# Performance work log

Hardware: AMD Instinct MI355X
Metric: run time of the kernel (lower is better)

Reference implementation:

```python
import jax, jax.numpy as jnp
import numpy as np

C = 256
C8 = C // 8
B, H, W = 4, 64, 64


def setup_inputs() -> dict:
    key = jax.random.key(0)
    ks = jax.random.split(key, 10)
    s = lambda fan_in: 1.0 / np.sqrt(fan_in)
    return {
        "x": jax.random.normal(ks[0], (B, C, H, W), dtype=jnp.float32),
        "conv_w": jax.random.normal(ks[1], (C8, C), dtype=jnp.float32) * s(C),
        "conv_b": jax.random.normal(ks[2], (C8,), dtype=jnp.float32) * 0.01,
        "q_w": jax.random.normal(ks[3], (C8, C8), dtype=jnp.float32) * s(C8),
        "q_b": jax.random.normal(ks[4], (C8,), dtype=jnp.float32) * 0.01,
        "k_w": jax.random.normal(ks[5], (C8, C8), dtype=jnp.float32) * s(C8),
        "k_b": jax.random.normal(ks[6], (C8,), dtype=jnp.float32) * 0.01,
        "v_w": jax.random.normal(ks[7], (C, C8), dtype=jnp.float32) * s(C8),
        "v_b": jax.random.normal(ks[8], (C,), dtype=jnp.float32) * 0.01,
        "gamma": jax.random.normal(ks[9], (1,), dtype=jnp.float32) * 0.1,
    }


def reference(x, conv_w, conv_b, q_w, q_b, k_w, k_b, v_w, v_b, gamma):
    b, c, h, w = x.shape
    hw = h * w
    # 1x1 convs are channel-mixing matmuls over flattened spatial dims
    xf = x.reshape(b, c, hw)                                   # [B, C, HW]
    proj = jnp.einsum('dc,bcn->bdn', conv_w, xf) + conv_b[None, :, None]   # [B, C8, HW]
    q = jnp.einsum('ed,bdn->bne', q_w, proj) + q_b[None, None, :]          # [B, HW, C8]
    k = jnp.einsum('ed,bdn->ben', k_w, proj) + k_b[None, :, None]          # [B, C8, HW]
    v = jnp.einsum('cd,bdn->bcn', v_w, proj) + v_b[None, :, None]          # [B, C, HW]
    attn = jax.nn.softmax(jnp.einsum('bne,bem->bnm', q, k), axis=-1)       # [B, HW, HW]
    out = jnp.einsum('bcm,bnm->bcn', v, attn)                              # [B, C, HW]
    out = out.reshape(b, c, h, w)
    return gamma[0] * out + x
```

## Files before the change

### kernel.cpp

```cpp
#include <hip/hip_runtime.h>
#include <hip/hip_bf16.h>
#include <stdint.h>

#define B_   4
#define C_   256
#define C8_  32
#define HW_  4096
#define ROWS_ 320
#define MS_  4
#define L2E  1.4426950408889634f

typedef __attribute__((ext_vector_type(8)))  short  short8;
typedef __attribute__((ext_vector_type(8)))  ushort us8;
typedef __attribute__((ext_vector_type(2)))  float  f32x2;
typedef __attribute__((ext_vector_type(16))) float  f32x16;

#define WT_OFF    0
#define BALL_OFF  (256*320*4)
#define Q_OFF     (BALL_OFF + 1280)
#define KT_OFF    (Q_OFF  + B_*HW_*C8_*2)
#define V_OFF     (KT_OFF + B_*HW_*C8_*2)
#define PACC_OFF  (V_OFF  + B_*C_*HW_*2)
#define LPART_OFF (PACC_OFF + (size_t)MS_*B_*C_*HW_*2)

__device__ __forceinline__ ushort f2bf(float f) {
    union { float f; uint32_t u; } v; v.f = f;
    uint32_t u = v.u;
    uint32_t r = u + 0x7fffu + ((u >> 16) & 1u);
    return (ushort)(r >> 16);
}
__device__ __forceinline__ uint32_t pktr(float lo, float hi) {
    union { float f; uint32_t u; } a, b; a.f = lo; b.f = hi;
    return __builtin_amdgcn_perm(b.u, a.u, 0x07060302u);
}
__device__ __forceinline__ uint32_t fexp2_pk(float s0, float s1, f32x2& e01) {
    f32x2 s = {s0, s1};
    f32x2 y = __builtin_elementwise_fma(s, (f32x2)(8388608.0f),
                                        (f32x2)(1064992506.0f));
    y = __builtin_elementwise_max(y, (f32x2)(0.0f));
    union { int i; float f; } c0, c1;
    c0.i = (int)y.x;  c1.i = (int)y.y;
    e01.x = c0.f;  e01.y = c1.f;
    return __builtin_amdgcn_perm((uint32_t)c1.i, (uint32_t)c0.i, 0x07060302u);
}

__global__ __launch_bounds__(256) void k_setup(
    const float* __restrict__ conv_w, const float* __restrict__ conv_b,
    const float* __restrict__ q_w, const float* __restrict__ q_b,
    const float* __restrict__ k_w, const float* __restrict__ k_b,
    const float* __restrict__ v_w, const float* __restrict__ v_b,
    ushort* __restrict__ wbf, float* __restrict__ ball)
{
    int r = blockIdx.x;
    int c = threadIdx.x;
    const float* wrow;
    float bias;
    if (r < 32)       { wrow = q_w + r*32;      bias = q_b[r];      }
    else if (r < 64)  { wrow = k_w + (r-32)*32; bias = k_b[r-32];   }
    else              { wrow = v_w + (r-64)*32; bias = v_b[r-64];   }
    float acc = 0.f;
    #pragma unroll
    for (int d = 0; d < 32; ++d) acc += wrow[d] * conv_w[d*C_ + c];
    float scale = (r < 32) ? L2E : 1.0f;
    int lanew = (r & 31) + 32*((c >> 3) & 1);
    int fidx  = (c >> 4)*10 + (r >> 5);
    wbf[fidx*512 + lanew*8 + (c & 7)] = f2bf(acc * scale);
    if (c == 0) {
        float bb = bias;
        #pragma unroll
        for (int d = 0; d < 32; ++d) bb += wrow[d] * conv_b[d];
        ball[r] = bb * scale;
    }
}

__global__ __launch_bounds__(320) void k_qkv(
    const float* __restrict__ x, const ushort* __restrict__ wbf,
    const float* __restrict__ ball,
    ushort* __restrict__ qg, ushort* __restrict__ ktg, ushort* __restrict__ vg)
{
    __shared__ float  xt[256*32];
    __shared__ ushort tr[5][32*40];

    int blk = blockIdx.x;
    int b  = blk >> 7;
    int nt = blk & 127;
    int n0 = nt * 32;
    int t = threadIdx.x;
    int w = t >> 6, lane = t & 63;
    int l31 = lane & 31, h = lane >> 5;

    const float* xsrc = x + (size_t)b*C_*HW_ + n0;
    if (w < 4) {
        #pragma unroll
        for (int i = 0; i < 8; ++i) {
            int chunk = w*8 + i;
            const float* src = xsrc + (size_t)(chunk*8 + (lane >> 3))*HW_
                               + (lane & 7)*4;
            __builtin_amdgcn_global_load_lds(
                (const __attribute__((address_space(1))) uint32_t*)src,
                (__attribute__((address_space(3))) uint32_t*)&xt[chunk*256],
                16, 0, 0);
        }
    }
    __syncthreads();

    f32x16 acc[2];
    acc[0] = (f32x16)(0.f);
    acc[1] = (f32x16)(0.f);

    #pragma unroll 4
    for (int kc = 0; kc < 16; ++kc) {
        short8 a0 = *(const short8*)(wbf + (kc*10 + w*2    )*512 + lane*8);
        short8 a1 = *(const short8*)(wbf + (kc*10 + w*2 + 1)*512 + lane*8);
        float xv[8];
        #pragma unroll
        for (int j = 0; j < 8; ++j)
            xv[j] = xt[kc*512 + (h*8 + j)*32 + l31];
        union { uint32_t d[4]; short8 s8; } bf;
        #pragma unroll
        for (int j2 = 0; j2 < 4; ++j2) bf.d[j2] = pktr(xv[2*j2], xv[2*j2+1]);
        acc[0] = __builtin_amdgcn_mfma_f32_32x32x16_bf16(a0, bf.s8, acc[0], 0, 0, 0);
        acc[1] = __builtin_amdgcn_mfma_f32_32x32x16_bf16(a1, bf.s8, acc[1], 0, 0, 0);
    }

    #pragma unroll
    for (int mi = 0; mi < 2; ++mi) {
        int rowb = w*64 + mi*32;
        bool isQK = (rowb < 64);
        #pragma unroll
        for (int r = 0; r < 16; ++r) {
            int roff = (r & 3) + 8*(r >> 2) + 4*h;
            ushort bv = f2bf(acc[mi][r] + ball[rowb + roff]);
            int ad = isQK ? (l31*40 + roff) : (roff*40 + l31);
            tr[w][ad] = bv;
        }
        __syncthreads();
        #pragma unroll
        for (int f = 0; f < 2; ++f) {
            us8 frag = *(const us8*)(&tr[w][l31*40 + f*16 + h*8]);
            if (isQK) {
                ushort* dstb = (rowb == 0) ? qg : ktg;
                size_t ad = ((size_t)((b*128 + nt)*2 + f) << 9) + lane*8;
                *(us8*)(dstb + ad) = frag;
            } else {
                int cblk = (rowb - 64) >> 5;
                int mb = nt*2 + f;
                size_t ad = ((size_t)((b*8 + cblk)*256 + mb) << 9) + lane*8;
                *(us8*)(vg + ad) = frag;
            }
        }
        __syncthreads();
    }
}

__global__ __launch_bounds__(512, 4) void k_attn(
    const ushort* __restrict__ qg, const ushort* __restrict__ ktg,
    const ushort* __restrict__ vg,
    ushort* __restrict__ pacc, float* __restrict__ lpart)
{
    __shared__ ushort v_lds[2][16*512];
    __shared__ ushort kt_lds[2][4*512];

    int blk = blockIdx.x;
    int ms = blk & 3;
    int cs = (blk >> 2) & 1;
    int qb = (blk >> 3) & 15;
    int b  = blk >> 7;
    int t = threadIdx.x;
    int w = t >> 6, lane = t & 63;
    int l31 = lane & 31, h = lane >> 5;
    int mbase = ms*1024;

    short8 qf[2];
    #pragma unroll
    for (int ks = 0; ks < 2; ++ks)
        qf[ks] = *(const short8*)(qg
            + ((size_t)((b*128 + qb*8 + w)*2 + ks) << 9) + lane*8);

    f32x16 acc[4];
    #pragma unroll
    for (int j = 0; j < 4; ++j) acc[j] = (f32x16)(0.f);
    f32x2 lacc0 = {0.f, 0.f};
    f32x2 lacc1 = {0.f, 0.f};

    #define STAGE(buf, m0)                                                          \
    {                                                                               \
        _Pragma("unroll")                                                           \
        for (int ff = 0; ff < 2; ++ff) {                                            \
            int f = w*2 + ff;                                                       \
            int cfr = f >> 2, mf = f & 3;                                           \
            const ushort* src = vg + ((size_t)((b*8 + cs*4 + cfr)*256               \
                                 + ((m0) >> 4) + mf) << 9) + lane*8;                \
            __builtin_amdgcn_global_load_lds(                                       \
                (const __attribute__((address_space(1))) uint32_t*)src,             \
                (__attribute__((address_space(3))) uint32_t*)&v_lds[buf][f*512],    \
                16, 0, 0);                                                          \
        }                                                                           \
        if (w < 4) {                                                                \
            const ushort* src = ktg + ((size_t)((b*128 + ((m0) >> 5) + (w >> 1))*2  \
                                 + (w & 1)) << 9) + lane*8;                         \
            __builtin_amdgcn_global_load_lds(                                       \
                (const __attribute__((address_space(1))) uint32_t*)src,             \
                (__attribute__((address_space(3))) uint32_t*)&kt_lds[buf][w*512],   \
                16, 0, 0);                                                          \
        }                                                                           \
    }

    #define PMERGE(uu, lo8, hi8)                                                    \
    {                                                                               \
        union { uint32_t d[4]; short8 s8; } fe_, fo_;                               \
        auto r02 = __builtin_amdgcn_permlane32_swap((int)uu[0], (int)uu[2], false, false); \
        auto r13 = __builtin_amdgcn_permlane32_swap((int)uu[1], (int)uu[3], false, false); \
        auto r46 = __builtin_amdgcn_permlane32_swap((int)uu[4], (int)uu[6], false, false); \
        auto r57 = __builtin_amdgcn_permlane32_swap((int)uu[5], (int)uu[7], false, false); \
        fe_.d[0] = (uint32_t)r02[0];  fe_.d[1] = (uint32_t)r13[0];                  \
        fe_.d[2] = (uint32_t)r02[1];  fe_.d[3] = (uint32_t)r13[1];                  \
        fo_.d[0] = (uint32_t)r46[0];  fo_.d[1] = (uint32_t)r57[0];                  \
        fo_.d[2] = (uint32_t)r46[1];  fo_.d[3] = (uint32_t)r57[1];                  \
        lo8 = fe_.s8;  hi8 = fo_.s8;                                               \
    }

    STAGE(0, mbase)
    __syncthreads();

    int buf = 0;
    for (int it = 0; it < 16; ++it) {
        if (it + 1 < 16) STAGE(buf ^ 1, mbase + (it+1)*64)

        short8 kt0a = *(const short8*)(&kt_lds[buf][0*512 + lane*8]);
        short8 kt1a = *(const short8*)(&kt_lds[buf][1*512 + lane*8]);
        f32x16 s_a = (f32x16)(0.f);
        __builtin_amdgcn_s_setprio(1);
        s_a = __builtin_amdgcn_mfma_f32_32x32x16_bf16(kt0a, qf[0], s_a, 0, 0, 0);
        s_a = __builtin_amdgcn_mfma_f32_32x32x16_bf16(kt1a, qf[1], s_a, 0, 0, 0);
        __builtin_amdgcn_s_setprio(0);

        uint32_t ua[8];
        #pragma unroll
        for (int i = 0; i < 8; ++i) {
            f32x2 e01;
            ua[i] = fexp2_pk(s_a[2*i], s_a[2*i+1], e01);
            if (i & 1) lacc1 += e01; else lacc0 += e01;
        }
        short8 pfa0, pfa1;
        PMERGE(ua, pfa0, pfa1)

        short8 kt0b = *(const short8*)(&kt_lds[buf][2*512 + lane*8]);
        short8 kt1b = *(const short8*)(&kt_lds[buf][3*512 + lane*8]);
        f32x16 s_b = (f32x16)(0.f);
        s_b = __builtin_amdgcn_mfma_f32_32x32x16_bf16(kt0b, qf[0], s_b, 0, 0, 0);
        s_b = __builtin_amdgcn_mfma_f32_32x32x16_bf16(kt1b, qf[1], s_b, 0, 0, 0);

        uint32_t ub[8];
        #pragma unroll
        for (int i = 0; i < 8; ++i) {
            f32x2 e01;
            ub[i] = fexp2_pk(s_b[2*i], s_b[2*i+1], e01);
            if (i & 1) lacc1 += e01; else lacc0 += e01;
        }
        #pragma unroll
        for (int msub = 0; msub < 2; ++msub) {
            short8 pfm = msub ? pfa1 : pfa0;
            int ks16 = msub;
            #pragma unroll
            for (int cfr = 0; cfr < 4; ++cfr) {
                short8 vf = *(const short8*)(&v_lds[buf][(cfr*4 + ks16)*512 + lane*8]);
                acc[cfr] = __builtin_amdgcn_mfma_f32_32x32x16_bf16(vf, pfm, acc[cfr], 0, 0, 0);
            }
        }
        short8 pfb0, pfb1;
        PMERGE(ub, pfb0, pfb1)

        __builtin_amdgcn_s_setprio(1);
        #pragma unroll
        for (int msub = 0; msub < 2; ++msub) {
            short8 pfm = msub ? pfb1 : pfb0;
            int ks16 = 2 + msub;
            #pragma unroll
            for (int cfr = 0; cfr < 4; ++cfr) {
                short8 vf = *(const short8*)(&v_lds[buf][(cfr*4 + ks16)*512 + lane*8]);
                acc[cfr] = __builtin_amdgcn_mfma_f32_32x32x16_bf16(vf, pfm, acc[cfr], 0, 0, 0);
            }
        }
        __builtin_amdgcn_s_setprio(0);

        __syncthreads();
        buf ^= 1;
    }

    f32x2 lacc = lacc0 + lacc1;
    float lsum = lacc.x + lacc.y;
    {
        union { float f; int i; } cv; cv.f = lsum;
        cv.i = __shfl_xor(cv.i, 32);
        lsum += cv.f;
    }
    if (cs == 0 && h == 0)
        lpart[(size_t)(ms*B_ + b)*HW_ + qb*256 + w*32 + l31] = lsum;

    int blkl = ((ms*B_ + b)*16 + qb)*2 + cs;
    #pragma unroll
    for (int cfr = 0; cfr < 4; ++cfr) {
        union { uint32_t d[8]; us8 hlf[2]; } pk;
        #pragma unroll
        for (int i = 0; i < 8; ++i)
            pk.d[i] = pktr(acc[cfr][2*i], acc[cfr][2*i+1]);
        ushort* dst = pacc + ((size_t)(blkl*32 + w*4 + cfr) << 10);
        *(us8*)(dst + lane*8)       = pk.hlf[0];
        *(us8*)(dst + 512 + lane*8) = pk.hlf[1];
    }
    #undef STAGE
    #undef PMERGE
}

__global__ __launch_bounds__(256) void k_comb(
    const ushort* __restrict__ pacc, const float* __restrict__ lpart,
    const float* __restrict__ x, const float* __restrict__ gamma_p,
    float* __restrict__ out)
{
    __shared__ float lds_acc[128*36];

    int blk = blockIdx.x;
    int w  = blk & 7;
    int cs = (blk >> 3) & 1;
    int qb = (blk >> 4) & 15;
    int b  = blk >> 8;
    int t = threadIdx.x;

    int l31 = t & 31;
    int h   = (t >> 5) & 1;
    int cfr = (t >> 6) & 3;
    int q = qb*256 + w*32 + l31;
    int lanef = h*32 + l31;

    float sum[16];
    #pragma unroll
    for (int k = 0; k < 16; ++k) sum[k] = 0.f;
    float lt = 0.f;

    #pragma unroll
    for (int ms = 0; ms < MS_; ++ms) {
        int blkl = ((ms*B_ + b)*16 + qb)*2 + cs;
        const ushort* pp = pacc + ((size_t)(blkl*32 + w*4 + cfr) << 10) + lanef*8;
        us8 a0 = *(const us8*)pp;
        us8 a1 = *(const us8*)(pp + 512);
        #pragma unroll
        for (int k = 0; k < 8; ++k) {
            union { uint32_t u; float f; } cv;
            cv.u = ((uint32_t)a0[k]) << 16;  sum[k]   += cv.f;
            cv.u = ((uint32_t)a1[k]) << 16;  sum[k+8] += cv.f;
        }
        lt += lpart[(size_t)(ms*B_ + b)*HW_ + q];
    }

    float rl = gamma_p[0] / lt;
    #pragma unroll
    for (int k = 0; k < 16; ++k) {
        int c = cfr*32 + (k & 3) + 8*(k >> 2) + 4*h;
        lds_acc[c*36 + l31] = sum[k]*rl;
    }
    __syncthreads();

    const float* xb = x + ((size_t)(b*C_ + cs*128))*HW_ + qb*256 + w*32;
    float* ob = out + ((size_t)(b*C_ + cs*128))*HW_ + qb*256 + w*32;
    #pragma unroll
    for (int i = 0; i < 4; ++i) {
        int s = t + i*256;
        int c = s >> 3, qg = s & 7;
        float4 a = *(const float4*)(&lds_acc[c*36 + qg*4]);
        size_t off = (size_t)c*HW_ + qg*4;
        float4 xv = *(const float4*)(xb + off);
        a.x += xv.x; a.y += xv.y; a.z += xv.z; a.w += xv.w;
        *(float4*)(ob + off) = a;
    }
}

extern "C" void kernel_launch(void* const* d_in, const int* in_sizes, int n_in,
                              void* d_out, int out_size, void* d_ws, size_t ws_size,
                              hipStream_t stream)
{
    const float* x      = (const float*)d_in[0];
    const float* conv_w = (const float*)d_in[1];
    const float* conv_b = (const float*)d_in[2];
    const float* q_w    = (const float*)d_in[3];
    const float* q_b    = (const float*)d_in[4];
    const float* k_w    = (const float*)d_in[5];
    const float* k_b    = (const float*)d_in[6];
    const float* v_w    = (const float*)d_in[7];
    const float* v_b    = (const float*)d_in[8];
    const float* gamma  = (const float*)d_in[9];
    float* out = (float*)d_out;

    char* ws = (char*)d_ws;
    ushort* wbf   = (ushort*)(ws + WT_OFF);
    float*  ball  = (float*)(ws + BALL_OFF);
    ushort* qg    = (ushort*)(ws + Q_OFF);
    ushort* ktg   = (ushort*)(ws + KT_OFF);
    ushort* vg    = (ushort*)(ws + V_OFF);
    ushort* pacc  = (ushort*)(ws + PACC_OFF);
    float*  lpart = (float*)(ws + LPART_OFF);

    k_setup<<<ROWS_, 256, 0, stream>>>(conv_w, conv_b, q_w, q_b, k_w, k_b,
                                       v_w, v_b, wbf, ball);
    k_qkv<<<B_*128, 320, 0, stream>>>(x, wbf, ball, qg, ktg, vg);
    k_attn<<<512, 512, 0, stream>>>(qg, ktg, vg, pacc, lpart);
    k_comb<<<1024, 256, 0, stream>>>(pacc, lpart, x, gamma, out);
}
```

Measured before the change: 150.2 us.

## Drop split-K partials and fuse softmax normalization and residual into attention kernel

```diff
diff --git a/kernel.cpp b/kernel.cpp
--- a/kernel.cpp
+++ b/kernel.cpp
@@ -7,7 +7,6 @@
 #define C8_  32
 #define HW_  4096
 #define ROWS_ 320
-#define MS_  4
 #define L2E  1.4426950408889634f
 
 typedef __attribute__((ext_vector_type(8)))  short  short8;
@@ -20,8 +19,6 @@
 #define Q_OFF     (BALL_OFF + 1280)
 #define KT_OFF    (Q_OFF  + B_*HW_*C8_*2)
 #define V_OFF     (KT_OFF + B_*HW_*C8_*2)
-#define PACC_OFF  (V_OFF  + B_*C_*HW_*2)
-#define LPART_OFF (PACC_OFF + (size_t)MS_*B_*C_*HW_*2)
 
 __device__ __forceinline__ ushort f2bf(float f) {
     union { float f; uint32_t u; } v; v.f = f;
@@ -153,29 +150,28 @@
     }
 }
 
-__global__ __launch_bounds__(512, 4) void k_attn(
+__global__ __launch_bounds__(128, 4) void k_attn(
     const ushort* __restrict__ qg, const ushort* __restrict__ ktg,
     const ushort* __restrict__ vg,
-    ushort* __restrict__ pacc, float* __restrict__ lpart)
+    const float* __restrict__ x, const float* __restrict__ gamma_p,
+    float* __restrict__ out)
 {
-    __shared__ ushort v_lds[2][16*512];
-    __shared__ ushort kt_lds[2][4*512];
+    __shared__ ushort v_lds[2][8*512];
+    __shared__ ushort kt_lds[2][2*512];
 
     int blk = blockIdx.x;
-    int ms = blk & 3;
-    int cs = (blk >> 2) & 1;
-    int qb = (blk >> 3) & 15;
+    int qp = blk & 63;
+    int cs = (blk >> 6) & 1;
     int b  = blk >> 7;
     int t = threadIdx.x;
     int w = t >> 6, lane = t & 63;
     int l31 = lane & 31, h = lane >> 5;
-    int mbase = ms*1024;
 
     short8 qf[2];
     #pragma unroll
     for (int ks = 0; ks < 2; ++ks)
         qf[ks] = *(const short8*)(qg
-            + ((size_t)((b*128 + qb*8 + w)*2 + ks) << 9) + lane*8);
+            + ((size_t)((b*128 + qp*2 + w)*2 + ks) << 9) + lane*8);
 
     f32x16 acc[4];
     #pragma unroll
@@ -183,25 +179,25 @@
     f32x2 lacc0 = {0.f, 0.f};
     f32x2 lacc1 = {0.f, 0.f};
 
-    #define STAGE(buf, m0)                                                          \
+    #define STAGE(bi, kti)                                                          \
     {                                                                               \
         _Pragma("unroll")                                                           \
-        for (int ff = 0; ff < 2; ++ff) {                                            \
-            int f = w*2 + ff;                                                       \
-            int cfr = f >> 2, mf = f & 3;                                           \
+        for (int ff = 0; ff < 4; ++ff) {                                            \
+            int f = w*4 + ff;                                                       \
+            int cfr = f >> 1, mf = f & 1;                                           \
             const ushort* src = vg + ((size_t)((b*8 + cs*4 + cfr)*256               \
-                                 + ((m0) >> 4) + mf) << 9) + lane*8;                \
+                                 + (kti)*2 + mf) << 9) + lane*8;                    \
             __builtin_amdgcn_global_load_lds(                                       \
                 (const __attribute__((address_space(1))) uint32_t*)src,             \
-                (__attribute__((address_space(3))) uint32_t*)&v_lds[buf][f*512],    \
+                (__attribute__((address_space(3))) uint32_t*)&v_lds[bi][f*512],     \
                 16, 0, 0);                                                          \
         }                                                                           \
-        if (w < 4) {                                                                \
-            const ushort* src = ktg + ((size_t)((b*128 + ((m0) >> 5) + (w >> 1))*2  \
-                                 + (w & 1)) << 9) + lane*8;                         \
+        {                                                                           \
+            const ushort* src = ktg + ((size_t)((b*128 + (kti))*2 + w) << 9)        \
+                                 + lane*8;                                          \
             __builtin_amdgcn_global_load_lds(                                       \
                 (const __attribute__((address_space(1))) uint32_t*)src,             \
-                (__attribute__((address_space(3))) uint32_t*)&kt_lds[buf][w*512],   \
+                (__attribute__((address_space(3))) uint32_t*)&kt_lds[bi][w*512],    \
                 16, 0, 0);                                                          \
         }                                                                           \
     }
@@ -220,65 +216,38 @@
         lo8 = fe_.s8;  hi8 = fo_.s8;                                               \
     }
 
-    STAGE(0, mbase)
+    STAGE(0, 0)
     __syncthreads();
 
     int buf = 0;
-    for (int it = 0; it < 16; ++it) {
-        if (it + 1 < 16) STAGE(buf ^ 1, mbase + (it+1)*64)
-
-        short8 kt0a = *(const short8*)(&kt_lds[buf][0*512 + lane*8]);
-        short8 kt1a = *(const short8*)(&kt_lds[buf][1*512 + lane*8]);
-        f32x16 s_a = (f32x16)(0.f);
+    for (int it = 0; it < 128; ++it) {
+        if (it + 1 < 128) STAGE(buf ^ 1, it + 1)
+
+        short8 kt0 = *(const short8*)(&kt_lds[buf][0*512 + lane*8]);
+        short8 kt1 = *(const short8*)(&kt_lds[buf][1*512 + lane*8]);
+        f32x16 s = (f32x16)(0.f);
         __builtin_amdgcn_s_setprio(1);
-        s_a = __builtin_amdgcn_mfma_f32_32x32x16_bf16(kt0a, qf[0], s_a, 0, 0, 0);
-        s_a = __builtin_amdgcn_mfma_f32_32x32x16_bf16(kt1a, qf[1], s_a, 0, 0, 0);
+        s = __builtin_amdgcn_mfma_f32_32x32x16_bf16(kt0, qf[0], s, 0, 0, 0);
+        s = __builtin_amdgcn_mfma_f32_32x32x16_bf16(kt1, qf[1], s, 0, 0, 0);
         __builtin_amdgcn_s_setprio(0);
 
-        uint32_t ua[8];
+        uint32_t u[8];
         #pragma unroll
         for (int i = 0; i < 8; ++i) {
             f32x2 e01;
-            ua[i] = fexp2_pk(s_a[2*i], s_a[2*i+1], e01);
+            u[i] = fexp2_pk(s[2*i], s[2*i+1], e01);
             if (i & 1) lacc1 += e01; else lacc0 += e01;
         }
-        short8 pfa0, pfa1;
-        PMERGE(ua, pfa0, pfa1)
-
-        short8 kt0b = *(const short8*)(&kt_lds[buf][2*512 + lane*8]);
-        short8 kt1b = *(const short8*)(&kt_lds[buf][3*512 + lane*8]);
-        f32x16 s_b = (f32x16)(0.f);
-        s_b = __builtin_amdgcn_mfma_f32_32x32x16_bf16(kt0b, qf[0], s_b, 0, 0, 0);
-        s_b = __builtin_amdgcn_mfma_f32_32x32x16_bf16(kt1b, qf[1], s_b, 0, 0, 0);
-
-        uint32_t ub[8];
-        #pragma unroll
-        for (int i = 0; i < 8; ++i) {
-            f32x2 e01;
-            ub[i] = fexp2_pk(s_b[2*i], s_b[2*i+1], e01);
-            if (i & 1) lacc1 += e01; else lacc0 += e01;
-        }
+        short8 pf0, pf1;
+        PMERGE(u, pf0, pf1)
+
+        __builtin_amdgcn_s_setprio(1);
         #pragma unroll
         for (int msub = 0; msub < 2; ++msub) {
-            short8 pfm = msub ? pfa1 : pfa0;
-            int ks16 = msub;
+            short8 pfm = msub ? pf1 : pf0;
             #pragma unroll
             for (int cfr = 0; cfr < 4; ++cfr) {
-                short8 vf = *(const short8*)(&v_lds[buf][(cfr*4 + ks16)*512 + lane*8]);
-                acc[cfr] = __builtin_amdgcn_mfma_f32_32x32x16_bf16(vf, pfm, acc[cfr], 0, 0, 0);
-            }
-        }
-        short8 pfb0, pfb1;
-        PMERGE(ub, pfb0, pfb1)
-
-        __builtin_amdgcn_s_setprio(1);
-        #pragma unroll
-        for (int msub = 0; msub < 2; ++msub) {
-            short8 pfm = msub ? pfb1 : pfb0;
-            int ks16 = 2 + msub;
-            #pragma unroll
-            for (int cfr = 0; cfr < 4; ++cfr) {
-                short8 vf = *(const short8*)(&v_lds[buf][(cfr*4 + ks16)*512 + lane*8]);
+                short8 vf = *(const short8*)(&v_lds[buf][(cfr*2 + msub)*512 + lane*8]);
                 acc[cfr] = __builtin_amdgcn_mfma_f32_32x32x16_bf16(vf, pfm, acc[cfr], 0, 0, 0);
             }
         }
@@ -295,84 +264,22 @@
         cv.i = __shfl_xor(cv.i, 32);
         lsum += cv.f;
     }
-    if (cs == 0 && h == 0)
-        lpart[(size_t)(ms*B_ + b)*HW_ + qb*256 + w*32 + l31] = lsum;
-
-    int blkl = ((ms*B_ + b)*16 + qb)*2 + cs;
+    float rl = gamma_p[0] / lsum;
+
+    int q = qp*64 + w*32 + l31;
+    const float* xb = x + (size_t)b*C_*HW_ + q;
+    float* ob = out + (size_t)b*C_*HW_ + q;
     #pragma unroll
     for (int cfr = 0; cfr < 4; ++cfr) {
-        union { uint32_t d[8]; us8 hlf[2]; } pk;
-        #pragma unroll
-        for (int i = 0; i < 8; ++i)
-            pk.d[i] = pktr(acc[cfr][2*i], acc[cfr][2*i+1]);
-        ushort* dst = pacc + ((size_t)(blkl*32 + w*4 + cfr) << 10);
-        *(us8*)(dst + lane*8)       = pk.hlf[0];
-        *(us8*)(dst + 512 + lane*8) = pk.hlf[1];
+        #pragma unroll
+        for (int i = 0; i < 16; ++i) {
+            int c = cs*128 + cfr*32 + (i & 3) + 8*(i >> 2) + 4*h;
+            size_t off = (size_t)c*HW_;
+            ob[off] = acc[cfr][i]*rl + xb[off];
+        }
     }
     #undef STAGE
     #undef PMERGE
-}
-
-__global__ __launch_bounds__(256) void k_comb(
-    const ushort* __restrict__ pacc, const float* __restrict__ lpart,
-    const float* __restrict__ x, const float* __restrict__ gamma_p,
-    float* __restrict__ out)
-{
-    __shared__ float lds_acc[128*36];
-
-    int blk = blockIdx.x;
-    int w  = blk & 7;
-    int cs = (blk >> 3) & 1;
-    int qb = (blk >> 4) & 15;
-    int b  = blk >> 8;
-    int t = threadIdx.x;
-
-    int l31 = t & 31;
-    int h   = (t >> 5) & 1;
-    int cfr = (t >> 6) & 3;
-    int q = qb*256 + w*32 + l31;
-    int lanef = h*32 + l31;
-
-    float sum[16];
-    #pragma unroll
-    for (int k = 0; k < 16; ++k) sum[k] = 0.f;
-    float lt = 0.f;
-
-    #pragma unroll
-    for (int ms = 0; ms < MS_; ++ms) {
-        int blkl = ((ms*B_ + b)*16 + qb)*2 + cs;
-        const ushort* pp = pacc + ((size_t)(blkl*32 + w*4 + cfr) << 10) + lanef*8;
-        us8 a0 = *(const us8*)pp;
-        us8 a1 = *(const us8*)(pp + 512);
-        #pragma unroll
-        for (int k = 0; k < 8; ++k) {
-            union { uint32_t u; float f; } cv;
-            cv.u = ((uint32_t)a0[k]) << 16;  sum[k]   += cv.f;
-            cv.u = ((uint32_t)a1[k]) << 16;  sum[k+8] += cv.f;
-        }
-        lt += lpart[(size_t)(ms*B_ + b)*HW_ + q];
-    }
-
-    float rl = gamma_p[0] / lt;
-    #pragma unroll
-    for (int k = 0; k < 16; ++k) {
-        int c = cfr*32 + (k & 3) + 8*(k >> 2) + 4*h;
-        lds_acc[c*36 + l31] = sum[k]*rl;
-    }
-    __syncthreads();
-
-    const float* xb = x + ((size_t)(b*C_ + cs*128))*HW_ + qb*256 + w*32;
-    float* ob = out + ((size_t)(b*C_ + cs*128))*HW_ + qb*256 + w*32;
-    #pragma unroll
-    for (int i = 0; i < 4; ++i) {
-        int s = t + i*256;
-        int c = s >> 3, qg = s & 7;
-        float4 a = *(const float4*)(&lds_acc[c*36 + qg*4]);
-        size_t off = (size_t)c*HW_ + qg*4;
-        float4 xv = *(const float4*)(xb + off);
-        a.x += xv.x; a.y += xv.y; a.z += xv.z; a.w += xv.w;
-        *(float4*)(ob + off) = a;
-    }
 }
 
 extern "C" void kernel_launch(void* const* d_in, const int* in_sizes, int n_in,
@@ -397,12 +304,9 @@
     ushort* qg    = (ushort*)(ws + Q_OFF);
     ushort* ktg   = (ushort*)(ws + KT_OFF);
     ushort* vg    = (ushort*)(ws + V_OFF);
-    ushort* pacc  = (ushort*)(ws + PACC_OFF);
-    float*  lpart = (float*)(ws + LPART_OFF);
 
     k_setup<<<ROWS_, 256, 0, stream>>>(conv_w, conv_b, q_w, q_b, k_w, k_b,
                                        v_w, v_b, wbf, ball);
     k_qkv<<<B_*128, 320, 0, stream>>>(x, wbf, ball, qg, ktg, vg);
-    k_attn<<<512, 512, 0, stream>>>(qg, ktg, vg, pacc, lpart);
-    k_comb<<<1024, 256, 0, stream>>>(pacc, lpart, x, gamma, out);
-}
+    k_attn<<<512, 128, 0, stream>>>(qg, ktg, vg, x, gamma, out);
+}
```

After: 208.3 us. +38.7%, slower.
